# Optimization experiments

Hardware: AMD Instinct MI355X
Metric: run time of the kernel (lower is better)

Reference implementation:

```python
import jax, jax.numpy as jnp
import numpy as np

B = 65536
IN_F = 1024
OUT_F = 1024
N_ACT = 4  # len(activation_functions): tanh, sin, relu, sigmoid (cyclic over columns)


def setup_inputs() -> dict:
    key = jax.random.key(0)
    k1, k2 = jax.random.split(key)
    x = jax.random.normal(k1, (B, IN_F), dtype=jnp.float32)
    # xavier_uniform for weight [out, in]
    limit = float(np.sqrt(6.0 / (IN_F + OUT_F)))
    W = jax.random.uniform(k2, (OUT_F, IN_F), dtype=jnp.float32, minval=-limit, maxval=limit)
    b = jnp.zeros((OUT_F,), dtype=jnp.float32)
    return {"input": x, "W": W, "b": b}


def _apply_cyclic_acts(y):
    # column i gets activation (i % N_ACT); OUT_F % N_ACT == 0 so reshape to groups
    Bb, O = y.shape
    yg = y.reshape(Bb, O // N_ACT, N_ACT)
    out = jnp.stack([
        jnp.tanh(yg[..., 0]),
        jnp.sin(yg[..., 1]),
        jax.nn.relu(yg[..., 2]),
        jax.nn.sigmoid(yg[..., 3]),
    ], axis=-1)
    return out.reshape(Bb, O)


def reference(input, W, b) -> jnp.ndarray:
    y = jnp.einsum('bi,oi->bo', input, W) + b  # F.linear
    return _apply_cyclic_acts(y)
```

## Files before the change

### kernel.cpp

```cpp
#include <hip/hip_runtime.h>

constexpr int B_ROWS = 65536;
constexpr int IN_F   = 1024;
constexpr int OUT_F  = 1024;

constexpr int BDIM = 256;
constexpr int BM = 128, BN = 128, BK = 32;

typedef __bf16 bf16x8 __attribute__((ext_vector_type(8)));
typedef float  f32x4  __attribute__((ext_vector_type(4)));

__device__ __forceinline__ bf16x8 cvt8(f32x4 u0, f32x4 u1) {
    bf16x8 v;
    v[0] = (__bf16)u0[0]; v[1] = (__bf16)u0[1]; v[2] = (__bf16)u0[2]; v[3] = (__bf16)u0[3];
    v[4] = (__bf16)u1[0]; v[5] = (__bf16)u1[1]; v[6] = (__bf16)u1[2]; v[7] = (__bf16)u1[3];
    return v;
}

__device__ __forceinline__ void glds16(const __bf16* g, unsigned char* l) {
    __builtin_amdgcn_global_load_lds(
        (const __attribute__((address_space(1))) unsigned int*)(const void*)g,
        (__attribute__((address_space(3))) unsigned int*)(void*)l,
        16, 0, 0);
}

#define BARC() asm volatile("s_waitcnt vmcnt(4) lgkmcnt(0)\n\ts_barrier" ::: "memory")
#define BAR0() asm volatile("s_waitcnt vmcnt(0) lgkmcnt(0)\n\ts_barrier" ::: "memory")

__global__ __launch_bounds__(256)
void cvt_bf16(const float* __restrict__ in, __bf16* __restrict__ out) {
    const size_t i = ((size_t)blockIdx.x * 256 + threadIdx.x) * 16;
    f32x4 a0 = *(const f32x4*)(in + i);
    f32x4 a1 = *(const f32x4*)(in + i + 4);
    f32x4 a2 = *(const f32x4*)(in + i + 8);
    f32x4 a3 = *(const f32x4*)(in + i + 12);
    *(bf16x8*)(out + i)     = cvt8(a0, a1);
    *(bf16x8*)(out + i + 8) = cvt8(a2, a3);
}

__global__ __launch_bounds__(BDIM, 3)
void fused_linear_act(const __bf16* __restrict__ Xb,
                      const __bf16* __restrict__ Wb,
                      const float* __restrict__ bias,
                      float* __restrict__ O)
{
    __shared__ __attribute__((aligned(16))) unsigned char lds[3 * 16384];

    const int bx  = blockIdx.x;
    const int xcd = bx & 7;
    const int idx = bx >> 3;
    const int nt  = idx & 7;
    const int mt  = xcd + 8 * (idx >> 3);
    const int m0 = mt * BM;
    const int n0 = nt * BN;

    const int tid  = threadIdx.x;
    const int lane = tid & 63;
    const int wave = tid >> 6;
    const int wm = (wave >> 1) * 64;
    const int wn = (wave & 1) * 64;
    const int lrow = lane & 15;
    const int quad = lane >> 4;

    f32x4 acc[4][4];
    #pragma unroll
    for (int i = 0; i < 4; ++i)
        #pragma unroll
        for (int j = 0; j < 4; ++j)
            acc[i][j] = (f32x4){0.f, 0.f, 0.f, 0.f};

    const __bf16* asrc0 = Xb + (size_t)(m0 + 16 * wave + lrow) * IN_F + quad * 8;
    const __bf16* asrc1 = asrc0 + (size_t)64 * IN_F;
    const __bf16* bsrc0 = Wb + (size_t)(n0 + 16 * wave + lrow) * IN_F + quad * 8;
    const __bf16* bsrc1 = bsrc0 + (size_t)64 * IN_F;
    const int wlds = wave * 1024;

    unsigned char* const buf0 = lds;
    unsigned char* const buf1 = lds + 16384;
    unsigned char* const buf2 = lds + 32768;

    const int rdAoff = (wm >> 4) * 1024 + lane * 16;
    const int rdBoff = 8192 + (wn >> 4) * 1024 + lane * 16;

    auto stage = [&](int koff, unsigned char* base) {
        glds16(asrc0 + koff, base + wlds);
        glds16(asrc1 + koff, base + wlds + 4096);
        glds16(bsrc0 + koff, base + 8192 + wlds);
        glds16(bsrc1 + koff, base + 8192 + wlds + 4096);
    };
    auto compute = [&](const unsigned char* base) {
        const unsigned char* ra = base + rdAoff;
        const unsigned char* rb = base + rdBoff;
        bf16x8 af[4], bfr[4];
        #pragma unroll
        for (int t = 0; t < 4; ++t) af[t]  = *(const bf16x8*)(ra + t * 1024);
        #pragma unroll
        for (int t = 0; t < 4; ++t) bfr[t] = *(const bf16x8*)(rb + t * 1024);
        #pragma unroll
        for (int i = 0; i < 4; ++i)
            #pragma unroll
            for (int j = 0; j < 4; ++j)
                acc[i][j] = __builtin_amdgcn_mfma_f32_16x16x32_bf16(af[i], bfr[j], acc[i][j], 0, 0, 0);
    };

    stage(0,  buf0);
    stage(32, buf1);

    int koff = 64;
    #pragma unroll 1
    for (int it = 0; it < 10; ++it) {
        BARC(); stage(koff, buf2); compute(buf0); koff += 32;
        BARC(); stage(koff, buf0); compute(buf1); koff += 32;
        BARC(); stage(koff, buf1); compute(buf2); koff += 32;
    }
    BARC(); compute(buf0);
    BAR0(); compute(buf1);

    const int s = lane & 3;
    const float kmul = (s == 0) ? -2.f : -1.f;
    const float aa   = (s == 0) ?  2.f :  1.f;
    const float cc   = (s == 0) ? -1.f :  0.f;
    const bool  is_sin  = (s == 1);
    const bool  is_relu = (s == 2);

    float bv[4];
    #pragma unroll
    for (int j = 0; j < 4; ++j) bv[j] = bias[n0 + wn + j * 16 + lrow];

    #pragma unroll
    for (int i = 0; i < 4; ++i) {
        #pragma unroll
        for (int r = 0; r < 4; ++r) {
            const int gr = m0 + wm + i * 16 + quad * 4 + r;
            float* op = O + (size_t)gr * OUT_F + n0 + wn + lrow;
            #pragma unroll
            for (int j = 0; j < 4; ++j) {
                const float y = acc[i][j][r] + bv[j];
                const float e = __expf(kmul * y);
                const float g = fmaf(aa, __builtin_amdgcn_rcpf(1.f + e), cc);
                const float sv = __sinf(y);
                const float rv = fmaxf(y, 0.f);
                const float res = is_sin ? sv : (is_relu ? rv : g);
                op[j * 16] = res;
            }
        }
    }
}

#define LDS_SYNC() asm volatile("s_waitcnt lgkmcnt(0)\n\ts_barrier" ::: "memory")
#define BAR_CNT() asm volatile("s_waitcnt vmcnt(4) lgkmcnt(0)\n\ts_barrier" ::: "memory")
#define BAR_ALL() asm volatile("s_waitcnt vmcnt(0) lgkmcnt(0)\n\ts_barrier" ::: "memory")

__global__ __launch_bounds__(BDIM, 4)
void fused_linear_act_f32a(const float* __restrict__ X,
                           const __bf16* __restrict__ Wb,
                           const float* __restrict__ bias,
                           float* __restrict__ O)
{
    __shared__ __attribute__((aligned(16))) unsigned char lds[2 * 16384];
    const int bx  = blockIdx.x;
    const int xcd = bx & 7;
    const int idx = bx >> 3;
    const int nt  = idx & 7;
    const int mt  = xcd + 8 * (idx >> 3);
    const int m0 = mt * BM;
    const int n0 = nt * BN;
    const int tid  = threadIdx.x;
    const int lane = tid & 63;
    const int wave = tid >> 6;
    const int wm = (wave >> 1) * 64;
    const int wn = (wave & 1) * 64;
    const int lrow = lane & 15;
    const int quad = lane >> 4;
    const int srow = tid >> 2;
    const int sseg = tid & 3;

    f32x4 acc[4][4];
    #pragma unroll
    for (int i = 0; i < 4; ++i)
        #pragma unroll
        for (int j = 0; j < 4; ++j)
            acc[i][j] = (f32x4){0.f, 0.f, 0.f, 0.f};

    const float* xa = X + (size_t)(m0 + srow) * IN_F + sseg * 8;
    const float* xb = xa + (size_t)64 * IN_F;
    const __bf16* wsrc0 = Wb + (size_t)(n0 + 16 * wave + lrow) * IN_F + quad * 8;
    const __bf16* wsrc1 = wsrc0 + (size_t)64 * IN_F;
    unsigned char* ldsB0 = lds + 8192 + wave * 1024;
    unsigned char* ldsB1 = ldsB0 + 4096;
    unsigned char* wr = &lds[((srow >> 4) * 64 + sseg * 16 + (srow & 15)) * 16];
    const unsigned char* rdA = &lds[(wm >> 4) * 1024 + lane * 16];
    const unsigned char* rdB = &lds[8192 + (wn >> 4) * 1024 + lane * 16];

    f32x4 A00 = *(const f32x4*)(xa);
    f32x4 A01 = *(const f32x4*)(xa + 4);
    f32x4 A10 = *(const f32x4*)(xb);
    f32x4 A11 = *(const f32x4*)(xb + 4);
    glds16(wsrc0, ldsB0);
    glds16(wsrc1, ldsB1);
    __builtin_amdgcn_sched_barrier(0);

    int koffA = 0, koffB = 0;
    auto stageA = [&](int buf) {
        unsigned char* w = wr + buf * 16384;
        *(bf16x8*)(w +    0) = cvt8(A00, A01);
        *(bf16x8*)(w + 4096) = cvt8(A10, A11);
        koffA = (koffA + BK) & (IN_F - 1);
        A00 = *(const f32x4*)(xa + koffA); A01 = *(const f32x4*)(xa + koffA + 4);
        A10 = *(const f32x4*)(xb + koffA); A11 = *(const f32x4*)(xb + koffA + 4);
    };
    auto stageB = [&](int buf) {
        koffB += BK;
        glds16(wsrc0 + koffB, ldsB0 + buf * 16384);
        glds16(wsrc1 + koffB, ldsB1 + buf * 16384);
        __builtin_amdgcn_sched_barrier(0);
    };
    auto compute = [&](int buf) {
        const unsigned char* ra = rdA + buf * 16384;
        const unsigned char* rb = rdB + buf * 16384;
        bf16x8 af[4], bfr[4];
        #pragma unroll
        for (int t = 0; t < 4; ++t) af[t]  = *(const bf16x8*)(ra + t * 1024);
        #pragma unroll
        for (int t = 0; t < 4; ++t) bfr[t] = *(const bf16x8*)(rb + t * 1024);
        #pragma unroll
        for (int i = 0; i < 4; ++i)
            #pragma unroll
            for (int j = 0; j < 4; ++j)
                acc[i][j] = __builtin_amdgcn_mfma_f32_16x16x32_bf16(af[i], bfr[j], acc[i][j], 0, 0, 0);
    };

    #pragma unroll 1
    for (int it = 0; it < IN_F / BK - 2; it += 2) {
        stageA(0); BAR_CNT(); stageB(1); compute(0);
        stageA(1); BAR_CNT(); stageB(0); compute(1);
    }
    stageA(0); BAR_CNT(); stageB(1); compute(0);
    stageA(1); BAR_ALL(); compute(1);

    const int s = lane & 3;
    const float kmul = (s == 0) ? -2.f : -1.f;
    const float aa   = (s == 0) ?  2.f :  1.f;
    const float cc   = (s == 0) ? -1.f :  0.f;
    const bool  is_sin  = (s == 1);
    const bool  is_relu = (s == 2);
    #pragma unroll
    for (int j = 0; j < 4; ++j) {
        const int gc = n0 + wn + j * 16 + lrow;
        const float bvv = bias[gc];
        #pragma unroll
        for (int i = 0; i < 4; ++i) {
            const int gr0 = m0 + wm + i * 16 + quad * 4;
            float* op = O + (size_t)gr0 * OUT_F + gc;
            #pragma unroll
            for (int r = 0; r < 4; ++r) {
                const float y = acc[i][j][r] + bvv;
                const float e = __expf(kmul * y);
                const float g = fmaf(aa, __builtin_amdgcn_rcpf(1.f + e), cc);
                const float sv = __sinf(y);
                const float rv = fmaxf(y, 0.f);
                const float res = is_sin ? sv : (is_relu ? rv : g);
                op[(size_t)r * OUT_F] = res;
            }
        }
    }
}

extern "C" void kernel_launch(void* const* d_in, const int* in_sizes, int n_in,
                              void* d_out, int out_size, void* d_ws, size_t ws_size,
                              hipStream_t stream) {
    const float* X = (const float*)d_in[0];
    const float* W = (const float*)d_in[1];
    const float* b = (const float*)d_in[2];
    float* O = (float*)d_out;

    const size_t nX = (size_t)B_ROWS * IN_F;
    const size_t nW = (size_t)OUT_F * IN_F;
    const size_t need = (nX + nW) * sizeof(__bf16);
    const int grid = (B_ROWS / BM) * (OUT_F / BN);

    if (ws_size >= need) {
        __bf16* Xb = (__bf16*)d_ws;
        __bf16* Wb = Xb + nX;
        cvt_bf16<<<(int)(nX / (256 * 16)), 256, 0, stream>>>(X, Xb);
        cvt_bf16<<<(int)(nW / (256 * 16)), 256, 0, stream>>>(W, Wb);
        fused_linear_act<<<grid, BDIM, 0, stream>>>(Xb, Wb, b, O);
    } else {
        __bf16* Wb = (__bf16*)d_ws;
        cvt_bf16<<<(int)(nW / (256 * 16)), 256, 0, stream>>>(W, Wb);
        fused_linear_act_f32a<<<grid, BDIM, 0, stream>>>(X, Wb, b, O);
    }
}
```

Measured before the change: 690.6 us.

## Enlarge GEMM tiles to 256x256x64 with 8 waves and interleaved prefetch schedule

```diff
diff --git a/kernel.cpp b/kernel.cpp
--- a/kernel.cpp
+++ b/kernel.cpp
@@ -4,8 +4,8 @@
 constexpr int IN_F   = 1024;
 constexpr int OUT_F  = 1024;
 
-constexpr int BDIM = 256;
-constexpr int BM = 128, BN = 128, BK = 32;
+constexpr int BDIM = 512;
+constexpr int BM = 256, BN = 256, BK = 64;
 
 typedef __bf16 bf16x8 __attribute__((ext_vector_type(8)));
 typedef float  f32x4  __attribute__((ext_vector_type(4)));
@@ -24,12 +24,15 @@
         16, 0, 0);
 }
 
-#define BARC() asm volatile("s_waitcnt vmcnt(4) lgkmcnt(0)\n\ts_barrier" ::: "memory")
-#define BAR0() asm volatile("s_waitcnt vmcnt(0) lgkmcnt(0)\n\ts_barrier" ::: "memory")
-
 __global__ __launch_bounds__(256)
-void cvt_bf16(const float* __restrict__ in, __bf16* __restrict__ out) {
-    const size_t i = ((size_t)blockIdx.x * 256 + threadIdx.x) * 16;
+void cvt_all(const float* __restrict__ X, const float* __restrict__ W,
+             __bf16* __restrict__ Xb, __bf16* __restrict__ Wb) {
+    const int b = blockIdx.x;
+    const float* in;
+    __bf16* out;
+    size_t i;
+    if (b < 16384) { in = X; out = Xb; i = ((size_t)b * 256 + threadIdx.x) * 16; }
+    else           { in = W; out = Wb; i = ((size_t)(b - 16384) * 256 + threadIdx.x) * 16; }
     f32x4 a0 = *(const f32x4*)(in + i);
     f32x4 a1 = *(const f32x4*)(in + i + 4);
     f32x4 a2 = *(const f32x4*)(in + i + 8);
@@ -38,83 +41,99 @@
     *(bf16x8*)(out + i + 8) = cvt8(a2, a3);
 }
 
-__global__ __launch_bounds__(BDIM, 3)
+__global__ __launch_bounds__(BDIM, 2)
 void fused_linear_act(const __bf16* __restrict__ Xb,
                       const __bf16* __restrict__ Wb,
                       const float* __restrict__ bias,
                       float* __restrict__ O)
 {
-    __shared__ __attribute__((aligned(16))) unsigned char lds[3 * 16384];
+    __shared__ __attribute__((aligned(16))) unsigned char lds[2 * 65536];
 
     const int bx  = blockIdx.x;
     const int xcd = bx & 7;
     const int idx = bx >> 3;
-    const int nt  = idx & 7;
-    const int mt  = xcd + 8 * (idx >> 3);
+    const int nt  = idx & 3;
+    const int mt  = xcd + 8 * (idx >> 2);
     const int m0 = mt * BM;
     const int n0 = nt * BN;
 
     const int tid  = threadIdx.x;
     const int lane = tid & 63;
     const int wave = tid >> 6;
-    const int wm = (wave >> 1) * 64;
-    const int wn = (wave & 1) * 64;
+    const int wr2  = wave >> 2;
+    const int w4   = wave & 3;
     const int lrow = lane & 15;
     const int quad = lane >> 4;
 
-    f32x4 acc[4][4];
-    #pragma unroll
-    for (int i = 0; i < 4; ++i)
+    const __bf16* agp = Xb + (size_t)(m0 + 32 * wave + lrow) * IN_F + quad * 8;
+    const __bf16* bgp = Wb + (size_t)(n0 + 32 * wave + lrow) * IN_F + quad * 8;
+
+    unsigned char* const b0 = lds;
+    unsigned char* const b1 = lds + 65536;
+
+    f32x4 acc[8][4];
+    #pragma unroll
+    for (int i = 0; i < 8; ++i)
         #pragma unroll
         for (int j = 0; j < 4; ++j)
             acc[i][j] = (f32x4){0.f, 0.f, 0.f, 0.f};
 
-    const __bf16* asrc0 = Xb + (size_t)(m0 + 16 * wave + lrow) * IN_F + quad * 8;
-    const __bf16* asrc1 = asrc0 + (size_t)64 * IN_F;
-    const __bf16* bsrc0 = Wb + (size_t)(n0 + 16 * wave + lrow) * IN_F + quad * 8;
-    const __bf16* bsrc1 = bsrc0 + (size_t)64 * IN_F;
-    const int wlds = wave * 1024;
-
-    unsigned char* const buf0 = lds;
-    unsigned char* const buf1 = lds + 16384;
-    unsigned char* const buf2 = lds + 32768;
-
-    const int rdAoff = (wm >> 4) * 1024 + lane * 16;
-    const int rdBoff = 8192 + (wn >> 4) * 1024 + lane * 16;
-
-    auto stage = [&](int koff, unsigned char* base) {
-        glds16(asrc0 + koff, base + wlds);
-        glds16(asrc1 + koff, base + wlds + 4096);
-        glds16(bsrc0 + koff, base + 8192 + wlds);
-        glds16(bsrc1 + koff, base + 8192 + wlds + 4096);
-    };
-    auto compute = [&](const unsigned char* base) {
-        const unsigned char* ra = base + rdAoff;
-        const unsigned char* rb = base + rdBoff;
-        bf16x8 af[4], bfr[4];
-        #pragma unroll
-        for (int t = 0; t < 4; ++t) af[t]  = *(const bf16x8*)(ra + t * 1024);
-        #pragma unroll
-        for (int t = 0; t < 4; ++t) bfr[t] = *(const bf16x8*)(rb + t * 1024);
-        #pragma unroll
-        for (int i = 0; i < 4; ++i)
-            #pragma unroll
-            for (int j = 0; j < 4; ++j)
-                acc[i][j] = __builtin_amdgcn_mfma_f32_16x16x32_bf16(af[i], bfr[j], acc[i][j], 0, 0, 0);
-    };
-
-    stage(0,  buf0);
-    stage(32, buf1);
-
-    int koff = 64;
+    bf16x8 aq0, aq1, aq2, aq3, bq0, bq1, bq2, bq3;
+
+#define GA(BUF, KH, K) do { unsigned char* _d = (BUF) + (KH) * 16384 + wave * 2048; \
+    glds16(agp + (K), _d); glds16(agp + (K) + 16 * IN_F, _d + 1024); } while (0)
+#define GB(BUF, KH, K) do { unsigned char* _d = (BUF) + 32768 + (KH) * 16384 + wave * 2048; \
+    glds16(bgp + (K), _d); glds16(bgp + (K) + 16 * IN_F, _d + 1024); } while (0)
+#define RA(BUF, KH, MH) do { \
+    const unsigned char* _r = (BUF) + (KH) * 16384 + (wr2 * 8 + (MH) * 4) * 1024 + lane * 16; \
+    aq0 = *(const bf16x8*)(_r);        aq1 = *(const bf16x8*)(_r + 1024); \
+    aq2 = *(const bf16x8*)(_r + 2048); aq3 = *(const bf16x8*)(_r + 3072); } while (0)
+#define RB(BUF, KH) do { \
+    const unsigned char* _r = (BUF) + 32768 + (KH) * 16384 + (w4 * 4) * 1024 + lane * 16; \
+    bq0 = *(const bf16x8*)(_r);        bq1 = *(const bf16x8*)(_r + 1024); \
+    bq2 = *(const bf16x8*)(_r + 2048); bq3 = *(const bf16x8*)(_r + 3072); } while (0)
+#define MFMA1(MH, I, J) acc[(MH)*4+(I)][(J)] = \
+    __builtin_amdgcn_mfma_f32_16x16x32_bf16(aq##I, bq##J, acc[(MH)*4+(I)][(J)], 0, 0, 0)
+#define MFMAQ(MH) do { __builtin_amdgcn_s_setprio(1); \
+    MFMA1(MH,0,0); MFMA1(MH,0,1); MFMA1(MH,0,2); MFMA1(MH,0,3); \
+    MFMA1(MH,1,0); MFMA1(MH,1,1); MFMA1(MH,1,2); MFMA1(MH,1,3); \
+    MFMA1(MH,2,0); MFMA1(MH,2,1); MFMA1(MH,2,2); MFMA1(MH,2,3); \
+    MFMA1(MH,3,0); MFMA1(MH,3,1); MFMA1(MH,3,2); MFMA1(MH,3,3); \
+    __builtin_amdgcn_s_setprio(0); } while (0)
+#define BAR() __builtin_amdgcn_s_barrier()
+#define VM4() asm volatile("s_waitcnt vmcnt(4)" ::: "memory")
+#define VM0() asm volatile("s_waitcnt vmcnt(0)" ::: "memory")
+
+#define ROUND_S(CUR, OPP, KT) do { \
+     GA(OPP, 1, ((KT) + 1) * 64 + 32); RB(CUR, 0); RA(CUR, 0, 0); \
+             BAR(); MFMAQ(0); BAR(); \
+     GB(OPP, 1, ((KT) + 1) * 64 + 32); RA(CUR, 0, 1); \
+             BAR(); MFMAQ(1); BAR(); \
+     GA(CUR, 0, ((KT) + 2) * 64); RB(CUR, 1); RA(CUR, 1, 0); \
+             BAR(); MFMAQ(0); BAR(); \
+     GB(CUR, 0, ((KT) + 2) * 64); RA(CUR, 1, 1); \
+             BAR(); MFMAQ(1); VM4(); BAR(); \
+} while (0)
+
+    GA(b0, 0, 0);  GB(b0, 0, 0);
+    GA(b0, 1, 32); GB(b0, 1, 32);
+    GA(b1, 0, 64); GB(b1, 0, 64);
+    VM4();
+    BAR();
+
     #pragma unroll 1
-    for (int it = 0; it < 10; ++it) {
-        BARC(); stage(koff, buf2); compute(buf0); koff += 32;
-        BARC(); stage(koff, buf0); compute(buf1); koff += 32;
-        BARC(); stage(koff, buf1); compute(buf2); koff += 32;
-    }
-    BARC(); compute(buf0);
-    BAR0(); compute(buf1);
+    for (int kt = 0; kt < 14; kt += 2) {
+        ROUND_S(b0, b1, kt);
+        ROUND_S(b1, b0, kt + 1);
+    }
+    GA(b1, 1, 15 * 64 + 32); RB(b0, 0); RA(b0, 0, 0); BAR(); MFMAQ(0); BAR();
+    GB(b1, 1, 15 * 64 + 32); RA(b0, 0, 1);            BAR(); MFMAQ(1); BAR();
+    RB(b0, 1); RA(b0, 1, 0);                          BAR(); MFMAQ(0); BAR();
+    RA(b0, 1, 1);                                     BAR(); MFMAQ(1); VM0(); BAR();
+    RB(b1, 0); RA(b1, 0, 0); BAR(); MFMAQ(0); BAR();
+    RA(b1, 0, 1);            BAR(); MFMAQ(1); BAR();
+    RB(b1, 1); RA(b1, 1, 0); BAR(); MFMAQ(0); BAR();
+    RA(b1, 1, 1);            BAR(); MFMAQ(1);
 
     const int s = lane & 3;
     const float kmul = (s == 0) ? -2.f : -1.f;
@@ -125,33 +144,44 @@
 
     float bv[4];
     #pragma unroll
-    for (int j = 0; j < 4; ++j) bv[j] = bias[n0 + wn + j * 16 + lrow];
-
-    #pragma unroll
-    for (int i = 0; i < 4; ++i) {
+    for (int fn = 0; fn < 4; ++fn) bv[fn] = bias[n0 + w4 * 64 + fn * 16 + lrow];
+
+    #pragma unroll
+    for (int fm = 0; fm < 8; ++fm) {
         #pragma unroll
         for (int r = 0; r < 4; ++r) {
-            const int gr = m0 + wm + i * 16 + quad * 4 + r;
-            float* op = O + (size_t)gr * OUT_F + n0 + wn + lrow;
+            const int gr = m0 + wr2 * 128 + fm * 16 + quad * 4 + r;
+            float* op = O + (size_t)gr * OUT_F + n0 + w4 * 64 + lrow;
             #pragma unroll
-            for (int j = 0; j < 4; ++j) {
-                const float y = acc[i][j][r] + bv[j];
+            for (int fn = 0; fn < 4; ++fn) {
+                const float y = acc[fm][fn][r] + bv[fn];
                 const float e = __expf(kmul * y);
                 const float g = fmaf(aa, __builtin_amdgcn_rcpf(1.f + e), cc);
                 const float sv = __sinf(y);
                 const float rv = fmaxf(y, 0.f);
                 const float res = is_sin ? sv : (is_relu ? rv : g);
-                op[j * 16] = res;
+                op[fn * 16] = res;
             }
         }
     }
 }
 
-#define LDS_SYNC() asm volatile("s_waitcnt lgkmcnt(0)\n\ts_barrier" ::: "memory")
-#define BAR_CNT() asm volatile("s_waitcnt vmcnt(4) lgkmcnt(0)\n\ts_barrier" ::: "memory")
-#define BAR_ALL() asm volatile("s_waitcnt vmcnt(0) lgkmcnt(0)\n\ts_barrier" ::: "memory")
-
-__global__ __launch_bounds__(BDIM, 4)
+constexpr int FBDIM = 256;
+#define FBAR_CNT() asm volatile("s_waitcnt vmcnt(4) lgkmcnt(0)\n\ts_barrier" ::: "memory")
+#define FBAR_ALL() asm volatile("s_waitcnt vmcnt(0) lgkmcnt(0)\n\ts_barrier" ::: "memory")
+
+__global__ __launch_bounds__(256)
+void w_to_bf16(const float* __restrict__ W, __bf16* __restrict__ Wb) {
+    const size_t i = ((size_t)blockIdx.x * 256 + threadIdx.x) * 16;
+    f32x4 a0 = *(const f32x4*)(W + i);
+    f32x4 a1 = *(const f32x4*)(W + i + 4);
+    f32x4 a2 = *(const f32x4*)(W + i + 8);
+    f32x4 a3 = *(const f32x4*)(W + i + 12);
+    *(bf16x8*)(Wb + i)     = cvt8(a0, a1);
+    *(bf16x8*)(Wb + i + 8) = cvt8(a2, a3);
+}
+
+__global__ __launch_bounds__(FBDIM, 4)
 void fused_linear_act_f32a(const float* __restrict__ X,
                            const __bf16* __restrict__ Wb,
                            const float* __restrict__ bias,
@@ -163,8 +193,8 @@
     const int idx = bx >> 3;
     const int nt  = idx & 7;
     const int mt  = xcd + 8 * (idx >> 3);
-    const int m0 = mt * BM;
-    const int n0 = nt * BN;
+    const int m0 = mt * 128;
+    const int n0 = nt * 128;
     const int tid  = threadIdx.x;
     const int lane = tid & 63;
     const int wave = tid >> 6;
@@ -205,12 +235,12 @@
         unsigned char* w = wr + buf * 16384;
         *(bf16x8*)(w +    0) = cvt8(A00, A01);
         *(bf16x8*)(w + 4096) = cvt8(A10, A11);
-        koffA = (koffA + BK) & (IN_F - 1);
+        koffA = (koffA + 32) & (IN_F - 1);
         A00 = *(const f32x4*)(xa + koffA); A01 = *(const f32x4*)(xa + koffA + 4);
         A10 = *(const f32x4*)(xb + koffA); A11 = *(const f32x4*)(xb + koffA + 4);
     };
     auto stageB = [&](int buf) {
-        koffB += BK;
+        koffB += 32;
         glds16(wsrc0 + koffB, ldsB0 + buf * 16384);
         glds16(wsrc1 + koffB, ldsB1 + buf * 16384);
         __builtin_amdgcn_sched_barrier(0);
@@ -231,12 +261,12 @@
     };
 
     #pragma unroll 1
-    for (int it = 0; it < IN_F / BK - 2; it += 2) {
-        stageA(0); BAR_CNT(); stageB(1); compute(0);
-        stageA(1); BAR_CNT(); stageB(0); compute(1);
-    }
-    stageA(0); BAR_CNT(); stageB(1); compute(0);
-    stageA(1); BAR_ALL(); compute(1);
+    for (int it = 0; it < IN_F / 32 - 2; it += 2) {
+        stageA(0); FBAR_CNT(); stageB(1); compute(0);
+        stageA(1); FBAR_CNT(); stageB(0); compute(1);
+    }
+    stageA(0); FBAR_CNT(); stageB(1); compute(0);
+    stageA(1); FBAR_ALL(); compute(1);
 
     const int s = lane & 3;
     const float kmul = (s == 0) ? -2.f : -1.f;
@@ -277,17 +307,19 @@
     const size_t nX = (size_t)B_ROWS * IN_F;
     const size_t nW = (size_t)OUT_F * IN_F;
     const size_t need = (nX + nW) * sizeof(__bf16);
-    const int grid = (B_ROWS / BM) * (OUT_F / BN);
 
     if (ws_size >= need) {
         __bf16* Xb = (__bf16*)d_ws;
         __bf16* Wb = Xb + nX;
-        cvt_bf16<<<(int)(nX / (256 * 16)), 256, 0, stream>>>(X, Xb);
-        cvt_bf16<<<(int)(nW / (256 * 16)), 256, 0, stream>>>(W, Wb);
+        const int xblocks = (int)(nX / (256 * 16));
+        const int wblocks = (int)(nW / (256 * 16));
+        cvt_all<<<xblocks + wblocks, 256, 0, stream>>>(X, W, Xb, Wb);
+        const int grid = (B_ROWS / BM) * (OUT_F / BN);
         fused_linear_act<<<grid, BDIM, 0, stream>>>(Xb, Wb, b, O);
     } else {
         __bf16* Wb = (__bf16*)d_ws;
-        cvt_bf16<<<(int)(nW / (256 * 16)), 256, 0, stream>>>(W, Wb);
-        fused_linear_act_f32a<<<grid, BDIM, 0, stream>>>(X, Wb, b, O);
-    }
-}
+        w_to_bf16<<<(int)(nW / (256 * 16)), 256, 0, stream>>>(W, Wb);
+        const int grid = (B_ROWS / 128) * (OUT_F / 128);
+        fused_linear_act_f32a<<<grid, FBDIM, 0, stream>>>(X, Wb, b, O);
+    }
+}
```

Result: faster. 599.7 us (-13.2%).
